# Optimization experiments

Measured on AMD Instinct MI355X. Metric: run time of the kernel, lower is better.

Reference implementation:

```python
import jax, jax.numpy as jnp
import numpy as np

D_STATE = 512


def _compute_ssm_matrices(S, K_raw, log_gamma, d_state):
    # K = K_raw / (sigma_max(K_raw).clamp(1e-5) + 0.002)  -- hard contraction
    sigma = jnp.linalg.norm(K_raw, ord=2)  # largest singular value
    sigma = jnp.maximum(sigma, 1e-5)
    K = K_raw / (sigma + 0.002)
    K11 = K[:d_state, :d_state]
    K12 = K[:d_state, d_state:]
    K21 = K[d_state:, :d_state]
    K22 = K[d_state:, d_state:]
    gamma = jnp.exp(log_gamma)
    Sinv = jnp.linalg.inv(S)
    A = Sinv @ K11 @ S
    B = gamma * (Sinv @ K12)
    C = K21 @ S
    D = gamma * K22
    return A, B, C, D


def setup_inputs() -> dict:
    key = jax.random.key(0)
    k1, k2, k3 = jax.random.split(key, 3)
    B_sz, T, H, N, P = 16, 4096, 512, 512, 512
    u = jax.random.normal(k1, (B_sz, T, H), dtype=jnp.float32)
    state = jnp.zeros((B_sz, N), dtype=jnp.float32)
    # S initialized as I + 0.01*randn (matches init_orthogonal_spectrum)
    S = jnp.eye(N, dtype=jnp.float32) + 0.01 * jax.random.normal(k2, (N, N), dtype=jnp.float32)
    K_raw = jax.random.normal(k3, (N + P, N + H), dtype=jnp.float32)
    log_gamma = jnp.zeros((), dtype=jnp.float32)  # gamma = 1.0
    return {"u": u, "state": state, "S": S, "K_raw": K_raw, "log_gamma": log_gamma}


def reference(u, state, S, K_raw, log_gamma):
    # u: [B,T,H], state: [B,N]
    A, Bm, C, D = _compute_ssm_matrices(S, K_raw, log_gamma, D_STATE)
    AT, BT, CT, DT = A.T, Bm.T, C.T, D.T

    def step(x, u_t):
        x_new = x @ AT + u_t @ BT  # [B,N]
        return x_new, x_new

    u_tbh = jnp.swapaxes(u, 0, 1)  # [T,B,H]
    _, xs = jax.lax.scan(step, state, u_tbh)  # xs: [T,B,N] = x_1..x_T
    states = jnp.concatenate([state[:, None, :], jnp.swapaxes(xs, 0, 1)], axis=1)  # [B,T+1,N]
    pre_states = states[:, :-1, :]  # x_0..x_{T-1}
    output = pre_states @ CT + u @ DT  # [B,T,d_output]
    return output, states
```

## Files before the change

### kernel.cpp

```cpp
#include <hip/hip_runtime.h>


typedef unsigned short u16;
typedef __bf16 bf16x8 __attribute__((ext_vector_type(8)));
typedef u16    u16x8  __attribute__((ext_vector_type(8)));
typedef float  f32x4  __attribute__((ext_vector_type(4)));

static_assert(sizeof(long) == 8, "need 64-bit long");

__device__ inline u16 f2bf(float f) {
    union { float f; unsigned u; } x; x.f = f;
    unsigned r = x.u + 0x7FFFu + ((x.u >> 16) & 1u);
    return (u16)(r >> 16);
}

__device__ inline bf16x8 cvt8(float4 v0, float4 v1) {
    bf16x8 a;
    a[0] = (__bf16)v0.x; a[1] = (__bf16)v0.y; a[2] = (__bf16)v0.z; a[3] = (__bf16)v0.w;
    a[4] = (__bf16)v1.x; a[5] = (__bf16)v1.y; a[6] = (__bf16)v1.z; a[7] = (__bf16)v1.w;
    return a;
}

__device__ inline void gl2lds16(const void* g, void* l) {
    auto gp = reinterpret_cast<const __attribute__((address_space(1))) char*>(
        (unsigned long long)g);
    auto lp = reinterpret_cast<__attribute__((address_space(3))) char*>(
        (unsigned)(unsigned long long)l);
    __builtin_amdgcn_global_load_lds(gp, lp, 16, 0, 0);
}

struct SArgs {
    const float* A1; long a1BS, a1RS; int a1Shift; unsigned a1Mask; int shiftA;
    int predLow; unsigned predMask;
    const float* A2; long a2BS, a2RS; int a2Shift; unsigned a2Mask;
    const u16* B1; const u16* B2;
    int K1c, Kc;
    const float* initP; long iBS, iRS; int iShift; unsigned iMask; float beta;
    float* Out; long oBS, oRS; int oShift; unsigned oMask;
    int sMode;
};

template<int MF>
__global__ __launch_bounds__(512, 4) void gemm_staged(SArgs g) {
    __shared__ char bstg[2][32768];
    const int tid = threadIdx.x, lane = tid & 63, wv = tid >> 6;
    const int kg = lane >> 4, l15 = lane & 15;
    const int rgw = wv >> 2, cg = wv & 3;
    const long row0 = (long)blockIdx.x * (32 * MF) + rgw * (16 * MF);
    const int cb = cg * 128;

    int Kc = g.Kc;
    const u16* B1 = g.B1;
    const u16* B2 = g.B2;
    float* Out = g.Out;
    if (g.sMode) {
        int s = blockIdx.z + 1;
        Kc = g.K1c + 16 * s;
        B1 = g.B1 + (long)(s - 1) * 262144;
        B2 = g.B2 + (long)(4 - s) * 262144;
        Out = g.Out + (long)s * 512;
    }
    const int K1c = g.K1c;

    const float* ap1[MF]; const float* ap2[MF]; bool pr[MF];
#pragma unroll
    for (int mf = 0; mf < MF; ++mf) {
        unsigned r = (unsigned)(row0 + mf * 16 + l15);
        pr[mf] = (g.predLow == 0) || ((r & g.predMask) >= (unsigned)g.predLow);
        long ra = (long)r - g.shiftA; if (ra < 0) ra = 0;
        ap1[mf] = g.A1 + ((ra >> g.a1Shift) * g.a1BS) + ((ra & (long)g.a1Mask) * g.a1RS) + kg * 8;
        ap2[mf] = nullptr;
        if (g.A2)
            ap2[mf] = g.A2 + (((long)(r >> g.a2Shift)) * g.a2BS) + ((long)(r & g.a2Mask) * g.a2RS) + kg * 8;
    }

    f32x4 acc[MF][8];
    if (g.initP) {
#pragma unroll
        for (int mf = 0; mf < MF; ++mf)
#pragma unroll
            for (int q = 0; q < 4; ++q) {
                unsigned r = (unsigned)(row0 + mf * 16 + kg * 4 + q);
                const float* ip = g.initP + ((long)(r >> g.iShift)) * g.iBS
                                + ((long)(r & g.iMask)) * g.iRS + cb + l15;
#pragma unroll
                for (int nf = 0; nf < 8; ++nf)
                    acc[mf][nf][q] = g.beta * ip[nf * 16];
            }
    } else {
#pragma unroll
        for (int mf = 0; mf < MF; ++mf)
#pragma unroll
            for (int nf = 0; nf < 8; ++nf)
                acc[mf][nf] = (f32x4){0.f, 0.f, 0.f, 0.f};
    }

    auto stage = [&](int c) {
        const char* src = (const char*)((c < K1c) ? (B1 + (long)c * 16384)
                                                  : (B2 + (long)(c - K1c) * 16384));
        char* dst = bstg[c & 1];
        const int wo = wv << 12;
#pragma unroll
        for (int i = 0; i < 4; ++i)
            gl2lds16(src + wo + (i << 10) + (lane << 4), dst + wo + (i << 10));
    };

    auto loadA = [&](int c, float4* v0, float4* v1) {
        if (c < K1c) {
#pragma unroll
            for (int mf = 0; mf < MF; ++mf) {
                v0[mf] = *(const float4*)(ap1[mf]);
                v1[mf] = *(const float4*)(ap1[mf] + 4);
                ap1[mf] += 32;
            }
        } else {
#pragma unroll
            for (int mf = 0; mf < MF; ++mf) {
                v0[mf] = *(const float4*)(ap2[mf]);
                v1[mf] = *(const float4*)(ap2[mf] + 4);
                ap2[mf] += 32;
            }
        }
    };

    auto body = [&](int c, float4* v0, float4* v1, int buf) {
        bf16x8 af[MF];
        bool mk = (c < K1c);
#pragma unroll
        for (int mf = 0; mf < MF; ++mf) {
            bf16x8 a = cvt8(v0[mf], v1[mf]);
            if (mk && !pr[mf]) { u16x8 z = {0,0,0,0,0,0,0,0}; a = __builtin_bit_cast(bf16x8, z); }
            af[mf] = a;
        }
        if (c + 2 < Kc) loadA(c + 2, v0, v1);

        const char* bb = bstg[buf] + kg * 8192 + (cb + l15) * 16;
#pragma unroll
        for (int nf = 0; nf < 8; ++nf) {
            u16x8 br = *(const u16x8*)(bb + nf * 256);
            bf16x8 bv = __builtin_bit_cast(bf16x8, br);
#pragma unroll
            for (int mf = 0; mf < MF; ++mf)
                acc[mf][nf] = __builtin_amdgcn_mfma_f32_16x16x32_bf16(af[mf], bv, acc[mf][nf], 0, 0, 0);
        }
        __syncthreads();
        if (c + 2 < Kc) stage(c + 2);
    };

    stage(0); stage(1);
    float4 a0v0[MF], a0v1[MF], a1v0[MF], a1v1[MF];
    loadA(0, a0v0, a0v1);
    loadA(1, a1v0, a1v1);
    __syncthreads();

    for (int c = 0; c < Kc; c += 2) {
        body(c,     a0v0, a0v1, 0);
        body(c + 1, a1v0, a1v1, 1);
    }

#pragma unroll
    for (int mf = 0; mf < MF; ++mf)
#pragma unroll
        for (int q = 0; q < 4; ++q) {
            unsigned r = (unsigned)(row0 + mf * 16 + kg * 4 + q);
            float* op = Out + ((long)(r >> g.oShift)) * g.oBS
                      + ((long)(r & g.oMask)) * g.oRS + cb + l15;
#pragma unroll
            for (int nf = 0; nf < 8; ++nf) op[nf * 16] = acc[mf][nf][q];
        }
}

struct GemmArgs {
    const float* A1; long a1RS; int shiftA;
    const u16*   Bp; long ldbN, colOff;
    const float* initP; long iRS; float beta;
    float* Out; long oRS;
    int Kit; int predLow;
    float* sumsq;
    const float* scalePtr; float cScale;
    u16* OutP; long opLd;
};

__global__ __launch_bounds__(256) void gemm_bf16(GemmArgs g) {
    const int lane = threadIdx.x & 63;
    const int wv   = threadIdx.x >> 6;
    const int kg   = lane >> 4;
    const int l15  = lane & 15;
    const unsigned row0 = blockIdx.x * 16;
    const long cb = (long)blockIdx.y * 512 + wv * 128;

    unsigned rA = row0 + l15;
    bool pr = (g.predLow == 0) || (rA >= (unsigned)g.predLow);
    long ra = (long)rA - g.shiftA; if (ra < 0) ra = 0;
    const float* ap = g.A1 + ra * g.a1RS + kg * 8;

    f32x4 acc[8];
#pragma unroll
    for (int nf = 0; nf < 8; ++nf) acc[nf] = (f32x4){0.f, 0.f, 0.f, 0.f};

    if (g.initP) {
#pragma unroll
        for (int q = 0; q < 4; ++q) {
            unsigned r = row0 + kg * 4 + q;
            const float* ip = g.initP + (long)r * g.iRS + cb + l15;
#pragma unroll
            for (int nf = 0; nf < 8; ++nf) acc[nf][q] = g.beta * ip[nf * 16];
        }
    }

    const u16* bp = g.Bp + ((long)kg * g.ldbN + g.colOff + cb + l15) * 8;
    const long bstep = g.ldbN * 32;

    for (int kk = 0; kk < g.Kit; ++kk) {
        float4 v0 = *(const float4*)(ap);
        float4 v1 = *(const float4*)(ap + 4);
        ap += 32;
        bf16x8 a = cvt8(v0, v1);
        if (!pr) { u16x8 z = {0,0,0,0,0,0,0,0}; a = __builtin_bit_cast(bf16x8, z); }
#pragma unroll
        for (int nf = 0; nf < 8; ++nf) {
            u16x8 braw = *(const u16x8*)(bp + (long)nf * 128);
            bf16x8 bb = __builtin_bit_cast(bf16x8, braw);
            acc[nf] = __builtin_amdgcn_mfma_f32_16x16x32_bf16(a, bb, acc[nf], 0, 0, 0);
        }
        bp += bstep;
    }

    float sc = g.cScale;
    if (g.scalePtr) sc *= 1.0f / g.scalePtr[0];
    float ss = 0.f;
#pragma unroll
    for (int q = 0; q < 4; ++q) {
        unsigned r = row0 + kg * 4 + q;
        float* op = g.Out + (long)r * g.oRS + cb + l15;
#pragma unroll
        for (int nf = 0; nf < 8; ++nf) {
            float v = sc * acc[nf][q];
            op[nf * 16] = v;
            ss += v * v;
            if (g.OutP) {
                long col = cb + l15 + nf * 16;
                g.OutP[((long)(r >> 3) * g.opLd + col) * 8 + (r & 7)] = f2bf(v);
            }
        }
    }
    if (g.sumsq) {
#pragma unroll
        for (int off = 32; off; off >>= 1) ss += __shfl_down(ss, off);
        if (lane == 0) atomicAdd(g.sumsq, ss);
    }
}

__global__ __launch_bounds__(256) void gemm_f32_512(const float* A, const float* B,
                                                    const float* I, float* O,
                                                    float alpha, float beta) {
    __shared__ float As[16][68];
    __shared__ float Bs[16][68];
    const int tx = threadIdx.x & 15, ty = threadIdx.x >> 4;
    const int bm = blockIdx.x * 64, bn = blockIdx.y * 64;
    float acc[4][4] = {};
    for (int k0 = 0; k0 < 512; k0 += 16) {
        for (int t = threadIdx.x; t < 1024; t += 256) {
            int r = t >> 4, c = t & 15;
            As[c][r] = A[(long)(bm + r) * 512 + k0 + c];
            int r2 = t >> 6, c2 = t & 63;
            Bs[r2][c2] = B[(long)(k0 + r2) * 512 + bn + c2];
        }
        __syncthreads();
#pragma unroll
        for (int k = 0; k < 16; ++k)
#pragma unroll
            for (int i = 0; i < 4; ++i)
#pragma unroll
                for (int j = 0; j < 4; ++j)
                    acc[i][j] += As[k][ty * 4 + i] * Bs[k][tx * 4 + j];
        __syncthreads();
    }
#pragma unroll
    for (int i = 0; i < 4; ++i)
#pragma unroll
        for (int j = 0; j < 4; ++j) {
            long o = (long)(bm + ty * 4 + i) * 512 + bn + tx * 4 + j;
            float v = alpha * acc[i][j];
            if (I) v += beta * I[o];
            O[o] = v;
        }
}

__global__ __launch_bounds__(256) void k_cast_panel(const float* src, long srcLd, long R, long C,
                                                    u16* panel, long pLd) {
    long total = R * C;
    for (long idx = (long)blockIdx.x * 256 + threadIdx.x; idx < total; idx += (long)gridDim.x * 256) {
        long k = idx / C, n = idx % C;
        panel[((k >> 3) * pLd + n) * 8 + (k & 7)] = f2bf(src[k * srcLd + n]);
    }
}

__global__ __launch_bounds__(256) void k_transpose_cast(const float* src, long srcLd, long R, long C,
                                                        u16* panel, long pLd, float* dstFT,
                                                        const float* slots, int sIdx) {
    float scale = (sIdx >= 0) ? slots[sIdx] : 1.0f;
    long total = R * C;
    for (long idx = (long)blockIdx.x * 256 + threadIdx.x; idx < total; idx += (long)gridDim.x * 256) {
        long i = idx / C, j = idx % C;
        float v = src[i * srcLd + j] * scale;
        if (panel) panel[((j >> 3) * pLd + i) * 8 + (j & 7)] = f2bf(v);
        if (dstFT) dstFT[j * R + i] = v;
    }
}

struct T4Args {
    const float* src0; const float* src1; const float* src2; const float* src3;
    long ld0, ld1, ld2, ld3;
    u16 *p0, *p1, *p2, *p3;
    float *f0, *f1, *f2, *f3;
    int s0, s1, s2, s3;
    const float* slots;
};
__global__ __launch_bounds__(256) void k_transpose4(T4Args t) {
    int m = blockIdx.y;
    const float* src; long ld; u16* panel; float* dstFT; int sIdx;
    if (m == 0) { src = t.src0; ld = t.ld0; panel = t.p0; dstFT = t.f0; sIdx = t.s0; }
    else if (m == 1) { src = t.src1; ld = t.ld1; panel = t.p1; dstFT = t.f1; sIdx = t.s1; }
    else if (m == 2) { src = t.src2; ld = t.ld2; panel = t.p2; dstFT = t.f2; sIdx = t.s2; }
    else { src = t.src3; ld = t.ld3; panel = t.p3; dstFT = t.f3; sIdx = t.s3; }
    float scale = (sIdx >= 0) ? t.slots[sIdx] : 1.0f;
    for (long idx = (long)blockIdx.x * 256 + threadIdx.x; idx < 262144; idx += (long)gridDim.x * 256) {
        long i = idx >> 9, j = idx & 511;
        float v = src[i * ld + j] * scale;
        panel[((j >> 3) * 512 + i) * 8 + (j & 7)] = f2bf(v);
        if (dstFT) dstFT[j * 512 + i] = v;
    }
}

__global__ __launch_bounds__(256) void k_sx1(const float* S, u16* Sp, float* Xf, u16* Xp) {
    for (long idx = (long)blockIdx.x * 256 + threadIdx.x; idx < 262144; idx += (long)gridDim.x * 256) {
        int i = (int)(idx >> 9), j = (int)(idx & 511);
        float sv = S[idx];
        Sp[(((long)(i >> 3)) * 512 + j) * 8 + (i & 7)] = f2bf(sv);
        float v = ((i == j) ? 2.0f : 0.0f) - sv;
        Xf[idx] = v;
        Xp[(((long)(i >> 3)) * 512 + j) * 8 + (i & 7)] = f2bf(v);
    }
}

__global__ void k_fin(float* slots, const float* lg) {
    float lnacc = 0.f, w = 1.f;
    for (int i = 0; i <= 8; ++i) {
        lnacc += w * 0.5f * logf(fmaxf(slots[i], 1e-30f));
        w *= 0.5f;
    }
    float sigma = fmaxf(expf(0.5f * lnacc), 1e-5f);
    float s = sigma + 0.002f;
    slots[32] = 1.0f / s;
    slots[33] = expf(lg[0]) / s;
}

__global__ __launch_bounds__(256) void k_state0(float* states, const float* state) {
    int i = blockIdx.x * 256 + threadIdx.x;
    if (i < 8192) {
        int b = i >> 9, n = i & 511;
        states[(long)b * 2097664 + n] = state[i];
    }
}

extern "C" void kernel_launch(void* const* d_in, const int* in_sizes, int n_in,
                              void* d_out, int out_size, void* d_ws, size_t ws_size,
                              hipStream_t stream) {
    (void)in_sizes; (void)n_in; (void)out_size; (void)ws_size;

    const float* u     = (const float*)d_in[0];
    const float* state = (const float*)d_in[1];
    const float* S     = (const float*)d_in[2];
    const float* K     = (const float*)d_in[3];
    const float* lg    = (const float*)d_in[4];

    float* out    = (float*)d_out;
    float* states = out + 33554432L;
    float* Zb     = out;

    char* w = (char*)d_ws;
    auto alloc = [&](size_t n) { void* p = w; w += (n + 255) & ~(size_t)255; return p; };
    float* slots = (float*)alloc(256);
    u16* Qall = (u16*)alloc(4L * 262144 * 2);
    u16* W4p  = (u16*)alloc(4L * 262144 * 2);
    u16* Q8p  = (u16*)alloc(262144L * 2);
    u16* Q16p = (u16*)alloc(262144L * 2);
    u16* CDT  = (u16*)alloc(2L * 262144 * 2);
    float* Qf   = (float*)alloc(4L * 262144 * 4);
    float* W4f  = (float*)alloc(4L * 262144 * 4);
    float* Q8f  = (float*)alloc(262144L * 4);
    float* Q16f = (float*)alloc(262144L * 4);
    float* Za   = (float*)w;
    float* KTf = (float*)alloc(1024L * 1024 * 4);
    u16*   Kp  = (u16*)  alloc(1024L * 1024 * 2);
    float* Mf  = (float*)alloc(1024L * 1024 * 4);
    u16*   Mp  = (u16*)  alloc(1024L * 1024 * 2);
    float* Mf2 = (float*)alloc(1024L * 1024 * 4);
    u16*   Mp2 = (u16*)  alloc(1024L * 1024 * 2);
    u16*   Sp  = (u16*)  alloc(512L * 512 * 2);
    float* Xaf = (float*)alloc(512L * 512 * 4);
    u16*   Xap = (u16*)  alloc(512L * 512 * 2);
    float* Xbf = (float*)alloc(512L * 512 * 4);
    u16*   Xbp = (u16*)  alloc(512L * 512 * 2);
    float* Pf  = (float*)alloc(512L * 512 * 4);
    u16*   Pp  = (u16*)  alloc(512L * 512 * 2);
    float* Xs  = (float*)alloc(512L * 512 * 4);
    float* T1f = (float*)alloc(512L * 512 * 4);
    u16*   T1p = (u16*)  alloc(512L * 512 * 2);
    float* Af  = (float*)alloc(512L * 512 * 4);
    float* Bmf = (float*)alloc(512L * 512 * 4);
    float* Cmf = (float*)alloc(512L * 512 * 4);

    auto mkargs = [&]() { GemmArgs a = {}; a.beta = 1.f; a.cScale = 1.f; return a; };
    auto launch_gemm = [&](int M, int N, const GemmArgs& a) {
        dim3 gr(M / 16, N / 512);
        gemm_bf16<<<gr, 256, 0, stream>>>(a);
    };

    hipMemsetAsync(slots, 0, 256, stream);

    k_transpose_cast<<<4096, 256, 0, stream>>>(K, 1024, 1024, 1024, nullptr, 0, KTf, nullptr, -1);
    k_cast_panel<<<4096, 256, 0, stream>>>(K, 1024, 1024, 1024, Kp, 1024);
    {   GemmArgs a = mkargs();
        a.A1 = KTf; a.a1RS = 1024;
        a.Bp = Kp; a.ldbN = 1024;
        a.Out = Mf; a.oRS = 1024; a.OutP = Mp; a.opLd = 1024;
        a.Kit = 32; a.sumsq = slots + 0;
        launch_gemm(1024, 1024, a);
    }
    {   float* Fs[2] = {Mf, Mf2};
        u16*   Ps[2] = {Mp, Mp2};
        for (int i = 1; i <= 8; ++i) {
            GemmArgs a = mkargs();
            a.A1 = Fs[(i + 1) & 1]; a.a1RS = 1024;
            a.Bp = Ps[(i + 1) & 1]; a.ldbN = 1024;
            a.Out = Fs[i & 1]; a.oRS = 1024; a.OutP = Ps[i & 1]; a.opLd = 1024;
            a.Kit = 32; a.sumsq = slots + i; a.scalePtr = slots + (i - 1);
            launch_gemm(1024, 1024, a);
        }
    }
    k_fin<<<1, 1, 0, stream>>>(slots, lg);

    k_sx1<<<1024, 256, 0, stream>>>(S, Sp, Xaf, Xap);
    float* curF = Xaf; u16* curP = Xap; float* nxtF = Xbf; u16* nxtP = Xbp;
    for (int it = 0; it < 3; ++it) {
        GemmArgs a = mkargs();
        a.A1 = S; a.a1RS = 512;
        a.Bp = curP; a.ldbN = 512;
        a.Out = Pf; a.oRS = 512; a.OutP = Pp; a.opLd = 512; a.cScale = -1.f;
        a.Kit = 16;
        launch_gemm(512, 512, a);
        GemmArgs b = mkargs();
        b.A1 = curF; b.a1RS = 512;
        b.Bp = Pp; b.ldbN = 512;
        b.initP = curF; b.iRS = 512; b.beta = 2.f;
        b.Out = nxtF; b.oRS = 512; b.OutP = nxtP; b.opLd = 512;
        b.Kit = 16;
        launch_gemm(512, 512, b);
        float* tf = curF; curF = nxtF; nxtF = tf;
        u16*   tp = curP; curP = nxtP; nxtP = tp;
    }
    gemm_f32_512<<<dim3(8, 8), 256, 0, stream>>>(S, curF, nullptr, Pf, 1.f, 0.f);
    gemm_f32_512<<<dim3(8, 8), 256, 0, stream>>>(curF, Pf, curF, Xs, -1.f, 2.f);

    {   GemmArgs a = mkargs();
        a.A1 = K; a.a1RS = 1024; a.Bp = Sp; a.ldbN = 512;
        a.Out = T1f; a.oRS = 512; a.OutP = T1p; a.opLd = 512; a.Kit = 16;
        launch_gemm(512, 512, a);
    }
    {   GemmArgs a = mkargs();
        a.A1 = Xs; a.a1RS = 512; a.Bp = T1p; a.ldbN = 512;
        a.Out = Af; a.oRS = 512; a.Kit = 16;
        launch_gemm(512, 512, a);
    }
    {   GemmArgs a = mkargs();
        a.A1 = Xs; a.a1RS = 512; a.Bp = Kp; a.ldbN = 1024; a.colOff = 512;
        a.Out = Bmf; a.oRS = 512; a.Kit = 16;
        launch_gemm(512, 512, a);
    }
    {   GemmArgs a = mkargs();
        a.A1 = K + 512L * 1024; a.a1RS = 1024; a.Bp = Sp; a.ldbN = 512;
        a.Out = Cmf; a.oRS = 512; a.Kit = 16;
        launch_gemm(512, 512, a);
    }
    {   T4Args t = {};
        t.src0 = Af;  t.ld0 = 512;  t.p0 = Qall;            t.f0 = Qf;            t.s0 = 32;
        t.src1 = Bmf; t.ld1 = 512;  t.p1 = W4p + 3*262144;  t.f1 = W4f + 3*262144; t.s1 = 33;
        t.src2 = Cmf; t.ld2 = 512;  t.p2 = CDT;             t.f2 = nullptr;       t.s2 = 32;
        t.src3 = K + 512L*1024 + 512; t.ld3 = 1024; t.p3 = CDT + 262144; t.f3 = nullptr; t.s3 = 33;
        t.slots = slots;
        k_transpose4<<<dim3(512, 4), 256, 0, stream>>>(t);
    }
    {   GemmArgs a = mkargs();
        a.A1 = Qf; a.a1RS = 512; a.Bp = Qall; a.ldbN = 512;
        a.Out = Qf + 262144; a.oRS = 512; a.OutP = Qall + 262144; a.opLd = 512; a.Kit = 16;
        launch_gemm(512, 512, a);
        a.A1 = Qf; a.Bp = Qall + 262144;
        a.Out = Qf + 2 * 262144; a.OutP = Qall + 2 * 262144;
        launch_gemm(1024, 512, a);
        a.A1 = Qf + 3 * 262144; a.Bp = Qall + 3 * 262144;
        a.Out = Q8f; a.OutP = Q8p;
        launch_gemm(512, 512, a);
        a.A1 = Q8f; a.Bp = Q8p;
        a.Out = Q16f; a.OutP = Q16p;
        launch_gemm(512, 512, a);
    }
    {   GemmArgs a = mkargs();
        a.A1 = W4f + 3 * 262144; a.a1RS = 512; a.Bp = Qall; a.ldbN = 512;
        a.Out = W4f + 2 * 262144; a.oRS = 512; a.OutP = W4p + 2 * 262144; a.opLd = 512; a.Kit = 16;
        launch_gemm(512, 512, a);
        a.A1 = W4f + 2 * 262144; a.Bp = Qall + 262144;
        a.Out = W4f; a.OutP = W4p;
        launch_gemm(1024, 512, a);
    }

    {   SArgs a = {};
        a.A1 = u; a.a1BS = 2097152; a.a1RS = 2048; a.a1Shift = 10; a.a1Mask = 1023;
        a.predMask = 1023;
        a.B1 = W4p; a.B2 = W4p; a.K1c = 64; a.Kc = 64;
        a.beta = 1.f;
        a.Out = Za; a.oBS = 0; a.oRS = 512; a.oShift = 14; a.oMask = 16383;
        gemm_staged<1><<<dim3(512, 1, 1), 512, 0, stream>>>(a);
    }
    {   GemmArgs f = mkargs();
        f.A1 = state; f.a1RS = 512;
        f.Bp = Qall + 3 * 262144; f.ldbN = 512;
        f.initP = Za; f.iRS = 524288; f.beta = 1.f;
        f.Out = Za; f.oRS = 524288; f.Kit = 16;
        launch_gemm(16, 512, f);
    }
    k_state0<<<32, 256, 0, stream>>>(states, state);

    auto ks = [&](const float* src, float* dst, int d, const u16* gen) {
        SArgs a = {};
        a.A1 = src; a.a1BS = 0; a.a1RS = 512; a.a1Shift = 14; a.a1Mask = 16383;
        a.shiftA = d; a.predLow = d; a.predMask = 1023;
        a.B1 = gen; a.B2 = gen; a.K1c = 16; a.Kc = 16;
        a.initP = src; a.iBS = 0; a.iRS = 512; a.iShift = 14; a.iMask = 16383; a.beta = 1.f;
        a.Out = dst; a.oBS = 0; a.oRS = 512; a.oShift = 14; a.oMask = 16383;
        gemm_staged<1><<<dim3(512, 1, 1), 512, 0, stream>>>(a);
    };
    ks(Za, Zb, 1, Qall + 3 * 262144);
    ks(Zb, Za, 2, Q8p);
    {
        SArgs a = {};
        a.A1 = Za; a.a1BS = 0; a.a1RS = 512; a.a1Shift = 14; a.a1Mask = 16383;
        a.shiftA = 4; a.predLow = 4; a.predMask = 1023;
        a.B1 = Q16p; a.B2 = Q16p; a.K1c = 16; a.Kc = 16;
        a.initP = Za; a.iBS = 0; a.iRS = 512; a.iShift = 14; a.iMask = 16383; a.beta = 1.f;
        a.Out = states + 2048; a.oBS = 2097664; a.oRS = 2048; a.oShift = 10; a.oMask = 1023;
        gemm_staged<1><<<dim3(512, 1, 1), 512, 0, stream>>>(a);
    }

    {   SArgs a = {};
        a.A1 = states; a.a1BS = 2097664; a.a1RS = 2048; a.a1Shift = 10; a.a1Mask = 1023;
        a.predMask = 1023;
        a.A2 = u; a.a2BS = 2097152; a.a2RS = 2048; a.a2Shift = 10; a.a2Mask = 1023;
        a.B1 = Qall; a.B2 = W4p; a.K1c = 16; a.Kc = 0;
        a.beta = 1.f;
        a.Out = states; a.oBS = 2097664; a.oRS = 2048; a.oShift = 10; a.oMask = 1023;
        a.sMode = 1;
        gemm_staged<2><<<dim3(256, 1, 3), 512, 0, stream>>>(a);
    }

    {   SArgs a = {};
        a.A1 = states; a.a1BS = 2097664; a.a1RS = 512; a.a1Shift = 12; a.a1Mask = 4095;
        a.predMask = 4095;
        a.A2 = u; a.a2BS = 2097152; a.a2RS = 512; a.a2Shift = 12; a.a2Mask = 4095;
        a.B1 = CDT; a.B2 = CDT + 262144; a.K1c = 16; a.Kc = 32;
        a.beta = 1.f;
        a.Out = out; a.oBS = 2097152; a.oRS = 512; a.oShift = 12; a.oMask = 4095;
        gemm_staged<2><<<dim3(1024, 1, 1), 512, 0, stream>>>(a);
    }
}
```

Before: 1.234 ms.

## Replace syncthreads with counted vmcnt waits and split small GEMM into single-wave blocks

In the staged GEMM, the full __syncthreads before each MFMA phase is replaced by explicit s_waitcnt vmcnt with a count that leaves the prefetched A loads in flight, plus raw s_barrier calls. The last two iterations are peeled so they can use smaller wait counts. This lets global A loads overlap the MFMA work instead of being drained at each barrier. Separately, the small gemm_bf16 kernel now launches 64-thread blocks covering 128 columns instead of 256-thread blocks covering 512, which gives more blocks for the small matrix prep GEMMs. The hand-counted vmcnt values depend on the exact order the compiler emits loads, so a wrong count could cause a race.

```diff
diff --git a/kernel.cpp b/kernel.cpp
--- a/kernel.cpp
+++ b/kernel.cpp
@@ -27,6 +27,15 @@
     auto lp = reinterpret_cast<__attribute__((address_space(3))) char*>(
         (unsigned)(unsigned long long)l);
     __builtin_amdgcn_global_load_lds(gp, lp, 16, 0, 0);
+}
+
+__device__ inline void wait_vmcnt(int n) {
+    switch (n) {
+        case 0:  asm volatile("s_waitcnt vmcnt(0)"  ::: "memory"); break;
+        case 6:  asm volatile("s_waitcnt vmcnt(6)"  ::: "memory"); break;
+        case 8:  asm volatile("s_waitcnt vmcnt(8)"  ::: "memory"); break;
+        default: asm volatile("s_waitcnt vmcnt(12)" ::: "memory"); break;
+    }
 }
 
 struct SArgs {
@@ -48,6 +57,7 @@
     const int rgw = wv >> 2, cg = wv & 3;
     const long row0 = (long)blockIdx.x * (32 * MF) + rgw * (16 * MF);
     const int cb = cg * 128;
+    constexpr int LA = 2 * MF;
 
     int Kc = g.Kc;
     const u16* B1 = g.B1;
@@ -123,7 +133,7 @@
         }
     };
 
-    auto body = [&](int c, float4* v0, float4* v1, int buf) {
+    auto body = [&](int c, float4* v0, float4* v1, int buf, int wn) {
         bf16x8 af[MF];
         bool mk = (c < K1c);
 #pragma unroll
@@ -134,6 +144,12 @@
         }
         if (c + 2 < Kc) loadA(c + 2, v0, v1);
 
+        __builtin_amdgcn_sched_barrier(0);
+        wait_vmcnt(wn);
+        __builtin_amdgcn_sched_barrier(0);
+        __builtin_amdgcn_s_barrier();
+        __builtin_amdgcn_sched_barrier(0);
+
         const char* bb = bstg[buf] + kg * 8192 + (cb + l15) * 16;
 #pragma unroll
         for (int nf = 0; nf < 8; ++nf) {
@@ -143,7 +159,12 @@
             for (int mf = 0; mf < MF; ++mf)
                 acc[mf][nf] = __builtin_amdgcn_mfma_f32_16x16x32_bf16(af[mf], bv, acc[mf][nf], 0, 0, 0);
         }
-        __syncthreads();
+
+        __builtin_amdgcn_sched_barrier(0);
+        asm volatile("s_waitcnt lgkmcnt(0)" ::: "memory");
+        __builtin_amdgcn_sched_barrier(0);
+        __builtin_amdgcn_s_barrier();
+        __builtin_amdgcn_sched_barrier(0);
         if (c + 2 < Kc) stage(c + 2);
     };
 
@@ -151,12 +172,13 @@
     float4 a0v0[MF], a0v1[MF], a1v0[MF], a1v1[MF];
     loadA(0, a0v0, a0v1);
     loadA(1, a1v0, a1v1);
-    __syncthreads();
-
-    for (int c = 0; c < Kc; c += 2) {
-        body(c,     a0v0, a0v1, 0);
-        body(c + 1, a1v0, a1v1, 1);
-    }
+
+    for (int c = 0; c + 4 <= Kc; c += 2) {
+        body(c,     a0v0, a0v1, 0, 2 * LA + 4);
+        body(c + 1, a1v0, a1v1, 1, 2 * LA + 4);
+    }
+    body(Kc - 2, a0v0, a0v1, 0, LA + 4);
+    body(Kc - 1, a1v0, a1v1, 1, 0);
 
 #pragma unroll
     for (int mf = 0; mf < MF; ++mf)
@@ -181,13 +203,12 @@
     u16* OutP; long opLd;
 };
 
-__global__ __launch_bounds__(256) void gemm_bf16(GemmArgs g) {
+__global__ __launch_bounds__(64) void gemm_bf16(GemmArgs g) {
     const int lane = threadIdx.x & 63;
-    const int wv   = threadIdx.x >> 6;
     const int kg   = lane >> 4;
     const int l15  = lane & 15;
     const unsigned row0 = blockIdx.x * 16;
-    const long cb = (long)blockIdx.y * 512 + wv * 128;
+    const long cb = (long)blockIdx.y * 128;
 
     unsigned rA = row0 + l15;
     bool pr = (g.predLow == 0) || (rA >= (unsigned)g.predLow);
@@ -414,8 +435,8 @@
 
     auto mkargs = [&]() { GemmArgs a = {}; a.beta = 1.f; a.cScale = 1.f; return a; };
     auto launch_gemm = [&](int M, int N, const GemmArgs& a) {
-        dim3 gr(M / 16, N / 512);
-        gemm_bf16<<<gr, 256, 0, stream>>>(a);
+        dim3 gr(M / 16, N / 128);
+        gemm_bf16<<<gr, 64, 0, stream>>>(a);
     };
 
     hipMemsetAsync(slots, 0, 256, stream);
```

Measured after the change: 1.428 ms. 15.7% more time.
